# Performance work log

Measured on AMD Instinct MI355X. Metric: run time of the kernel, lower is better.

## Reference

```python
import jax, jax.numpy as jnp
import numpy as np

B, N, C_IN = 16, 1024, 768
H, KQ, VD = 8, 256, 512          # num_heads, kq_dim, v_dim per head
NH_V = H * VD                    # 4096
D_OUT = 512
SCALE = D_OUT ** -0.5            # module uses dim_out**-0.5
EPS = 1e-5


def _bn(x, gamma, beta, mean, var):
    # eval-mode BatchNorm1d over last dim
    return (x - mean) * (gamma * jax.lax.rsqrt(var + EPS)) + beta


def setup_inputs() -> dict:
    key = jax.random.key(0)
    ks = jax.random.split(key, 8)
    return {
        "x": jax.random.normal(ks[0], (B, N, C_IN), jnp.float32),
        "qkv_w": jax.random.normal(ks[1], (2 * H * KQ + NH_V, C_IN), jnp.float32) * 0.02,
        "qkv_gamma": jax.random.uniform(ks[2], (2 * H * KQ + NH_V,), jnp.float32),
        "qkv_beta": jax.random.normal(ks[3], (2 * H * KQ + NH_V,), jnp.float32) * 0.02,
        "qkv_mean": jax.random.normal(ks[4], (2 * H * KQ + NH_V,), jnp.float32) * 0.02,
        "qkv_var": jnp.ones((2 * H * KQ + NH_V,), jnp.float32),
        "pos_bias": jax.random.normal(ks[5], (H, N, N), jnp.float32),
        "proj_w": jax.random.normal(ks[6], (D_OUT, NH_V), jnp.float32) * 0.02,
        "proj_gamma": jax.random.uniform(ks[7], (D_OUT,), jnp.float32),
        "proj_beta": jnp.zeros((D_OUT,), jnp.float32),
        "proj_mean": jnp.zeros((D_OUT,), jnp.float32),
        "proj_var": jnp.ones((D_OUT,), jnp.float32),
    }


def reference(x, qkv_w, qkv_gamma, qkv_beta, qkv_mean, qkv_var,
              pos_bias, proj_w, proj_gamma, proj_beta, proj_mean, proj_var):
    b, n, _ = x.shape
    qkv = _bn(x @ qkv_w.T, qkv_gamma, qkv_beta, qkv_mean, qkv_var)  # [B,N,h]
    qkv = qkv.reshape(b, n, H, 2 * KQ + VD)
    q, k, v = jnp.split(qkv, [KQ, 2 * KQ], axis=3)                  # [B,N,H,*]
    attn = jnp.einsum('bnhd,bmhd->bhnm', q, k) * SCALE + pos_bias   # [B,H,N,N]
    attn = jax.nn.softmax(attn, axis=-1)
    out = jnp.einsum('bhnm,bmhd->bnhd', attn, v).reshape(b, n, NH_V)
    out = jnp.clip(out, -1.0, 1.0)                                  # Hardtanh
    return _bn(out @ proj_w.T, proj_gamma, proj_beta, proj_mean, proj_var)
```

## Files before the change

### kernel.cpp

```cpp
#include <hip/hip_runtime.h>

using v8bf  = __bf16 __attribute__((ext_vector_type(8)));
using v16f  = float  __attribute__((ext_vector_type(16)));

#define EPS_BN 1e-5f
#define ATT_SCALE 0.044194173824159216f
#define KSPLIT 2

__device__ __forceinline__ unsigned short f2bf(float f){
  union { float f; unsigned int u; } c; c.f = f;
  unsigned int u = c.u + 0x7fffu + ((c.u >> 16) & 1u);
  return (unsigned short)(u >> 16);
}

__device__ __forceinline__ v8bf ld8(const unsigned short* p){
  union { uint4 u; v8bf v; } c;
  c.u = *(const uint4*)p;
  return c.v;
}

__device__ __forceinline__ void glds16(const unsigned short* g, unsigned short* l){
  __builtin_amdgcn_global_load_lds(
      (const __attribute__((address_space(1))) void*)g,
      (__attribute__((address_space(3))) void*)l, 16, 0, 0);
}

__global__ void cast_bf16_kernel(const float* __restrict__ src,
                                 unsigned short* __restrict__ dst, int n8){
  int i = blockIdx.x * 256 + threadIdx.x;
  if (i >= n8) return;
  const float4* s4 = (const float4*)src;
  float4 a = s4[2*i], b = s4[2*i+1];
  union { unsigned short s[8]; uint4 u; } r;
  r.s[0]=f2bf(a.x); r.s[1]=f2bf(a.y); r.s[2]=f2bf(a.z); r.s[3]=f2bf(a.w);
  r.s[4]=f2bf(b.x); r.s[5]=f2bf(b.y); r.s[6]=f2bf(b.z); r.s[7]=f2bf(b.w);
  ((uint4*)dst)[i] = r.u;
}

__global__ void bn_precompute(const float* __restrict__ g, const float* __restrict__ be,
                              const float* __restrict__ mn, const float* __restrict__ vr,
                              float* __restrict__ scale, float* __restrict__ shift,
                              int n, int qfold){
  int i = blockIdx.x * 256 + threadIdx.x;
  if (i >= n) return;
  float s = g[i] * rsqrtf(vr[i] + EPS_BN);
  float t = be[i] - mn[i] * s;
  if (qfold && (i & 1023) < 256){ s *= ATT_SCALE; t *= ATT_SCALE; }
  scale[i] = s; shift[i] = t;
}

template<int MODE>
__launch_bounds__(256, 2)
__global__ void gemm_nt(const unsigned short* __restrict__ A,
                        const unsigned short* __restrict__ Bm,
                        int K, long sA, long sB, long mbase,
                        const float* __restrict__ scale, const float* __restrict__ shift,
                        const float* __restrict__ sums,
                        unsigned short* __restrict__ ob16,
                        float* __restrict__ outf,
                        unsigned short* __restrict__ vt)
{
  __shared__ __align__(16) unsigned short Sh[16384];
  unsigned short* As = Sh;
  unsigned short* Bs = Sh + 8192;
  const int tid = threadIdx.x;
  const int w = tid >> 6, lane = tid & 63, ln = lane & 31, lg = lane >> 5;
  const int wm = (w >> 1) * 64, wn = (w & 1) * 64;
  const long bm = (long)blockIdx.y * 128, bn = (long)blockIdx.x * 128;
  const int z = blockIdx.z;
  const unsigned short* Ab = A + (MODE == 3 ? 0L : (long)z * sA) + bm * K;
  const unsigned short* Bb = Bm + (MODE == 3 ? 0L : (long)z * sB) + bn * K;

  const int kbeg = (MODE == 3) ? z * (K >> 2) : 0;
  const int kend = (MODE == 3) ? kbeg + (K >> 2) : K;

  const int rsub = lane >> 3;
  const int gsl  = lane & 7;
  const unsigned short* gA[4]; const unsigned short* gB[4];
  unsigned short *lA[4], *lB[4];
  #pragma unroll
  for (int i = 0; i < 4; i++){
    int r = w*32 + i*8 + rsub;
    int go = (gsl ^ (r & 7)) * 8;
    gA[i] = Ab + (long)r * K + go;
    gB[i] = Bb + (long)r * K + go;
    lA[i] = As + (w*32 + i*8) * 64;
    lB[i] = Bs + (w*32 + i*8) * 64;
  }

  v16f acc[2][2];
  #pragma unroll
  for (int a = 0; a < 2; a++)
    #pragma unroll
    for (int b = 0; b < 2; b++)
      #pragma unroll
      for (int i = 0; i < 16; i++) acc[a][b][i] = 0.f;

  for (int k0 = kbeg; k0 < kend; k0 += 64){
    __syncthreads();
    #pragma unroll
    for (int i = 0; i < 4; i++){
      glds16(gA[i] + k0, lA[i]);
      glds16(gB[i] + k0, lB[i]);
    }
    __syncthreads();
    #pragma unroll
    for (int kk = 0; kk < 4; kk++){
      v8bf af[2], bfr[2];
      #pragma unroll
      for (int t = 0; t < 2; t++){
        int Ra = wm + t*32 + ln;
        af[t] = *(const v8bf*)&As[Ra*64 + ((kk*2 + lg) ^ (Ra & 7))*8];
        int Rb = wn + t*32 + ln;
        bfr[t] = *(const v8bf*)&Bs[Rb*64 + ((kk*2 + lg) ^ (Rb & 7))*8];
      }
      #pragma unroll
      for (int tm = 0; tm < 2; tm++)
        #pragma unroll
        for (int tn = 0; tn < 2; tn++)
          acc[tm][tn] = __builtin_amdgcn_mfma_f32_32x32x16_bf16(af[tm], bfr[tn], acc[tm][tn], 0, 0, 0);
    }
  }

  if (MODE == 0 && (blockIdx.x & 4)){
    __syncthreads();
    unsigned short* Ts = Sh;
    #pragma unroll
    for (int tm = 0; tm < 2; tm++){
      #pragma unroll
      for (int tn = 0; tn < 2; tn++){
        int c = wn + tn*32 + ln;
        long gn = bn + c;
        float sc = scale[gn], sh = shift[gn];
        int xk = (c & 15) << 3;
        #pragma unroll
        for (int q = 0; q < 4; q++){
          int mq = wm + tm*32 + 8*q + 4*lg;
          union { unsigned short s[4]; unsigned long long u; } pk;
          #pragma unroll
          for (int j = 0; j < 4; j++)
            pk.s[j] = f2bf(acc[tm][tn][q*4 + j] * sc + sh);
          *(unsigned long long*)&Ts[c*128 + (mq ^ xk)] = pk.u;
        }
      }
    }
    __syncthreads();
    const int h  = (int)(bn >> 10);
    const int j0 = (int)(bn & 1023) - 512;
    unsigned short* Vtb = vt + ((bm >> 10)*8 + h) * 524288L;
    const int nl0 = (int)(bm & 1023);
    #pragma unroll
    for (int i = 0; i < 8; i++){
      int idx = i*256 + tid;
      int c = idx >> 4, g = idx & 15;
      uint4 u = *(const uint4*)&Ts[c*128 + ((g ^ (c & 15)) << 3)];
      *(uint4*)(Vtb + (long)(j0 + c)*1024 + nl0 + g*8) = u;
    }
    return;
  }

  float invs[2][16];
  if (MODE == 1){
    #pragma unroll
    for (int tm = 0; tm < 2; tm++)
      #pragma unroll
      for (int i = 0; i < 16; i++){
        long gm = bm + wm + tm*32 + (i&3) + 8*(i>>2) + 4*lg;
        const float* sp = sums + (long)z * (KSPLIT*1024L) + gm;
        float s = 0.f;
        #pragma unroll
        for (int kp = 0; kp < KSPLIT; kp++) s += sp[kp*1024];
        invs[tm][i] = 1.0f / s;
      }
  }

  #pragma unroll
  for (int tm = 0; tm < 2; tm++){
    #pragma unroll
    for (int tn = 0; tn < 2; tn++){
      long gn = bn + wn + tn*32 + ln;
      float sc = 0.f, sh = 0.f;
      if (MODE == 0){ sc = scale[gn]; sh = shift[gn]; }
      #pragma unroll
      for (int i = 0; i < 16; i++){
        long gm = bm + wm + tm*32 + (i&3) + 8*(i>>2) + 4*lg;
        float v = acc[tm][tn][i];
        if (MODE == 0){
          ob16[gm*8192 + gn] = f2bf(v * sc + sh);
        } else if (MODE == 1){
          v = v * invs[tm][i];
          v = fminf(1.f, fmaxf(-1.f, v));
          int b2 = z >> 3, hh = z & 7;
          ob16[((long)b2*1024 + gm)*4096 + hh*512 + gn] = f2bf(v);
        } else {
          outf[((long)z * mbase + gm)*512 + gn] = v;
        }
      }
    }
  }
}

__global__ void reduce_bn(const float* __restrict__ part,
                          const float* __restrict__ sc, const float* __restrict__ sh,
                          float* __restrict__ out, long Mtot, long mbase){
  long idx = (long)blockIdx.x * 256 + threadIdx.x;
  if (idx >= Mtot * 128) return;
  long gm = idx >> 7;
  int gn4 = (int)(idx & 127) * 4;
  long PS = Mtot * 512;
  const float* p = part + gm*512 + gn4;
  float4 p0 = *(const float4*)(p);
  float4 p1 = *(const float4*)(p + PS);
  float4 p2 = *(const float4*)(p + 2*PS);
  float4 p3 = *(const float4*)(p + 3*PS);
  float4 s4 = *(const float4*)(sc + gn4);
  float4 h4 = *(const float4*)(sh + gn4);
  float4 r;
  r.x = (p0.x+p1.x+p2.x+p3.x)*s4.x + h4.x;
  r.y = (p0.y+p1.y+p2.y+p3.y)*s4.y + h4.y;
  r.z = (p0.z+p1.z+p2.z+p3.z)*s4.z + h4.z;
  r.w = (p0.w+p1.w+p2.w+p3.w)*s4.w + h4.w;
  *(float4*)(out + (mbase + gm)*512 + gn4) = r;
}

__launch_bounds__(256, 2)
__global__ void attn_scores(const unsigned short* __restrict__ qkv,
                            const float* __restrict__ bias,
                            unsigned short* __restrict__ E,
                            float* __restrict__ psums)
{
  __shared__ __align__(16) unsigned short Ks[2][64*256];
  const int lid  = blockIdx.x + (blockIdx.y << 4);
  const int xcd  = lid & 7;
  const int s_   = lid >> 3;
  const int mblk = s_ & 15;
  const int bh   = xcd + 8 * (s_ >> 4);
  const int b2 = bh >> 3, h = bh & 7;
  const int tid = threadIdx.x, w = tid >> 6, lane = tid & 63, ln = lane & 31, lg = lane >> 5;
  const int mh = w & 1, kh = w >> 1;
  const int m0 = mblk * 64 + mh * 32;
  const unsigned short* qbase = qkv + (long)b2*1024*8192 + h*1024;
  const unsigned short* kbase = qbase + 256;
  const float* biash = bias + (long)h * 1048576;
  unsigned short* Eb = E + (long)bh * 1048576;

  v8bf qf[16];
  {
    const unsigned short* qrow = qbase + (long)(m0 + ln)*8192 + lg*8;
    #pragma unroll
    for (int kf = 0; kf < 16; kf++) qf[kf] = ld8(qrow + kf*16);
  }

  const int rr = lane >> 5, slot = lane & 31;

  float sm[16];
  #pragma unroll
  for (int i = 0; i < 16; i++) sm[i] = 0.f;

  const int NT = 16;

  #pragma unroll
  for (int i = 0; i < 8; i++){
    int row = w*16 + i*2 + rr;
    glds16(kbase + (long)row*8192 + (slot ^ (row & 31))*8, &Ks[0][(w*16 + i*2)*256]);
  }

  for (int tt = 0; tt < NT; tt++){
    __syncthreads();
    const int cb = tt & 1;

    const int col = tt*64 + kh*32 + ln;
    float br[16];
    #pragma unroll
    for (int q = 0; q < 4; q++)
      #pragma unroll
      for (int j = 0; j < 4; j++)
        br[q*4 + j] = biash[(long)(m0 + 4*lg + 8*q + j)*1024 + col];

    if (tt < NT - 1){
      const int nb = cb ^ 1;
      #pragma unroll
      for (int i = 0; i < 8; i++){
        int row = w*16 + i*2 + rr;
        glds16(kbase + (long)((tt+1)*64 + row)*8192 + (slot ^ (row & 31))*8,
               &Ks[nb][(w*16 + i*2)*256]);
      }
    }

    v16f a[4];
    #pragma unroll
    for (int c = 0; c < 4; c++)
      #pragma unroll
      for (int i = 0; i < 16; i++) a[c][i] = 0.f;
    #pragma unroll
    for (int kb = 0; kb < 16; kb++){
      v8bf kf8 = *(const v8bf*)&Ks[cb][(kh*32 + ln)*256 + ((2*kb + lg) ^ ln)*8];
      a[kb & 3] = __builtin_amdgcn_mfma_f32_32x32x16_bf16(qf[kb], kf8, a[kb & 3], 0, 0, 0);
    }

    #pragma unroll
    for (int q = 0; q < 4; q++){
      #pragma unroll
      for (int j = 0; j < 4; j++){
        int i = q*4 + j;
        int r = 4*lg + 8*q + j;
        float e = __expf((a[0][i] + a[1][i]) + (a[2][i] + a[3][i]) + br[i]);
        sm[i] += e;
        Eb[(long)(m0 + r)*1024 + col] = f2bf(e);
      }
    }
  }

  #pragma unroll
  for (int i = 0; i < 16; i++){
    #pragma unroll
    for (int d = 1; d < 32; d <<= 1) sm[i] += __shfl_xor(sm[i], d, 64);
  }
  if (ln == 0){
    float* sp = psums + ((long)bh * KSPLIT + kh)*1024 + m0 + 4*lg;
    #pragma unroll
    for (int q = 0; q < 4; q++)
      #pragma unroll
      for (int j = 0; j < 4; j++)
        sp[8*q + j] = sm[q*4 + j];
  }
}

extern "C" void kernel_launch(void* const* d_in, const int* in_sizes, int n_in,
                              void* d_out, int out_size, void* d_ws, size_t ws_size,
                              hipStream_t stream)
{
  const float* x        = (const float*)d_in[0];
  const float* qkv_w    = (const float*)d_in[1];
  const float* qg       = (const float*)d_in[2];
  const float* qb       = (const float*)d_in[3];
  const float* qm       = (const float*)d_in[4];
  const float* qv       = (const float*)d_in[5];
  const float* pos_bias = (const float*)d_in[6];
  const float* pw       = (const float*)d_in[7];
  const float* pg       = (const float*)d_in[8];
  const float* pbt      = (const float*)d_in[9];
  const float* pmn      = (const float*)d_in[10];
  const float* pvr      = (const float*)d_in[11];
  float* out = (float*)d_out;

  const unsigned long FIXED = 16846848UL;
  const unsigned long PERG  = 43548672UL;
  long G = 1;
  if      (ws_size >= FIXED + PERG*16) G = 16;
  else if (ws_size >= FIXED + PERG*8)  G = 8;
  else if (ws_size >= FIXED + PERG*4)  G = 4;
  else if (ws_size >= FIXED + PERG*2)  G = 2;
  else if (ws_size >= FIXED + PERG)    G = 1;
  else return;

  char* ws = (char*)d_ws;
  unsigned short* wqb = (unsigned short*)(ws + 0L);
  unsigned short* wpb = (unsigned short*)(ws + 12582912L);
  float* sc_qkv       = (float*)(ws + 16777216L);
  float* sh_qkv       = (float*)(ws + 16809984L);
  float* sc_p         = (float*)(ws + 16842752L);
  float* sh_p         = (float*)(ws + 16844800L);
  const long gb = 16846848L;
  unsigned short* xbg   = (unsigned short*)(ws + gb);
  unsigned short* qkvg  = (unsigned short*)(ws + gb + G*1572864L);
  unsigned short* Vtg   = (unsigned short*)(ws + gb + G*18350080L);
  unsigned short* Eg    = (unsigned short*)(ws + gb + G*26738688L);
  float* sumsg          = (float*)(ws + gb + G*43515904L);
  unsigned short* outcg = qkvg;
  float* partials       = (float*)Eg;
  float* psums          = (float*)xbg;
  (void)sumsg;

  cast_bf16_kernel<<<dim3(3072), 256, 0, stream>>>(qkv_w, wqb, 786432);
  cast_bf16_kernel<<<dim3(1024), 256, 0, stream>>>(pw,    wpb, 262144);
  bn_precompute<<<dim3(32), 256, 0, stream>>>(qg, qb, qm, qv, sc_qkv, sh_qkv, 8192, 1);
  bn_precompute<<<dim3(2),  256, 0, stream>>>(pg, pbt, pmn, pvr, sc_p, sh_p, 512, 0);

  const int nG = (int)(16 / G);
  for (int g = 0; g < nG; g++){
    const float* xg = x + (long)g * G * 786432L;
    long mbase = (long)g * G * 1024L;

    cast_bf16_kernel<<<dim3((unsigned)(G*384)), 256, 0, stream>>>(xg, xbg, (int)(G*98304));

    gemm_nt<0><<<dim3(64, (unsigned)(8*G), 1), 256, 0, stream>>>(
        xbg, wqb, 768, 0L, 0L, 0L, sc_qkv, sh_qkv, nullptr, qkvg, nullptr, Vtg);

    attn_scores<<<dim3(16, (unsigned)(8*G)), 256, 0, stream>>>(
        qkvg, pos_bias, Eg, psums);

    gemm_nt<1><<<dim3(4, 8, (unsigned)(8*G)), 256, 0, stream>>>(
        Eg, Vtg, 1024, 1048576L, 524288L, 0L, nullptr, nullptr, psums, outcg, nullptr, nullptr);

    gemm_nt<3><<<dim3(4, (unsigned)(8*G), 4), 256, 0, stream>>>(
        outcg, wpb, 4096, 0L, 0L, (long)(G*1024), nullptr, nullptr, nullptr,
        nullptr, partials, nullptr);

    reduce_bn<<<dim3((unsigned)(G*512)), 256, 0, stream>>>(
        partials, sc_p, sh_p, out, (long)(G*1024), mbase);
  }
}
```

Baseline: 979.5 us.

## Double-buffer LDS tiles in gemm_nt to overlap global loads with MFMA

```diff
diff --git a/kernel.cpp b/kernel.cpp
--- a/kernel.cpp
+++ b/kernel.cpp
@@ -60,9 +60,7 @@
                         float* __restrict__ outf,
                         unsigned short* __restrict__ vt)
 {
-  __shared__ __align__(16) unsigned short Sh[16384];
-  unsigned short* As = Sh;
-  unsigned short* Bs = Sh + 8192;
+  __shared__ __align__(16) unsigned short Sh[32768];
   const int tid = threadIdx.x;
   const int w = tid >> 6, lane = tid & 63, ln = lane & 31, lg = lane >> 5;
   const int wm = (w >> 1) * 64, wn = (w & 1) * 64;
@@ -77,15 +75,14 @@
   const int rsub = lane >> 3;
   const int gsl  = lane & 7;
   const unsigned short* gA[4]; const unsigned short* gB[4];
-  unsigned short *lA[4], *lB[4];
+  int lofs[4];
   #pragma unroll
   for (int i = 0; i < 4; i++){
     int r = w*32 + i*8 + rsub;
     int go = (gsl ^ (r & 7)) * 8;
     gA[i] = Ab + (long)r * K + go;
     gB[i] = Bb + (long)r * K + go;
-    lA[i] = As + (w*32 + i*8) * 64;
-    lB[i] = Bs + (w*32 + i*8) * 64;
+    lofs[i] = (w*32 + i*8) * 64;
   }
 
   v16f acc[2][2];
@@ -96,23 +93,35 @@
       #pragma unroll
       for (int i = 0; i < 16; i++) acc[a][b][i] = 0.f;
 
+  #pragma unroll
+  for (int i = 0; i < 4; i++){
+    glds16(gA[i] + kbeg, Sh + lofs[i]);
+    glds16(gB[i] + kbeg, Sh + 16384 + lofs[i]);
+  }
+  asm volatile("s_waitcnt vmcnt(0) lgkmcnt(0)" ::: "memory");
+  __builtin_amdgcn_s_barrier();
+
+  int cur = 0;
   for (int k0 = kbeg; k0 < kend; k0 += 64){
-    __syncthreads();
-    #pragma unroll
-    for (int i = 0; i < 4; i++){
-      glds16(gA[i] + k0, lA[i]);
-      glds16(gB[i] + k0, lB[i]);
-    }
-    __syncthreads();
+    if (k0 + 64 < kend){
+      const int nb = cur ^ 1;
+      #pragma unroll
+      for (int i = 0; i < 4; i++){
+        glds16(gA[i] + k0 + 64, Sh + nb*8192 + lofs[i]);
+        glds16(gB[i] + k0 + 64, Sh + 16384 + nb*8192 + lofs[i]);
+      }
+    }
+    const unsigned short* Ac = Sh + cur*8192;
+    const unsigned short* Bc = Sh + 16384 + cur*8192;
     #pragma unroll
     for (int kk = 0; kk < 4; kk++){
       v8bf af[2], bfr[2];
       #pragma unroll
       for (int t = 0; t < 2; t++){
         int Ra = wm + t*32 + ln;
-        af[t] = *(const v8bf*)&As[Ra*64 + ((kk*2 + lg) ^ (Ra & 7))*8];
+        af[t] = *(const v8bf*)&Ac[Ra*64 + ((kk*2 + lg) ^ (Ra & 7))*8];
         int Rb = wn + t*32 + ln;
-        bfr[t] = *(const v8bf*)&Bs[Rb*64 + ((kk*2 + lg) ^ (Rb & 7))*8];
+        bfr[t] = *(const v8bf*)&Bc[Rb*64 + ((kk*2 + lg) ^ (Rb & 7))*8];
       }
       #pragma unroll
       for (int tm = 0; tm < 2; tm++)
@@ -120,10 +129,12 @@
         for (int tn = 0; tn < 2; tn++)
           acc[tm][tn] = __builtin_amdgcn_mfma_f32_32x32x16_bf16(af[tm], bfr[tn], acc[tm][tn], 0, 0, 0);
     }
+    asm volatile("s_waitcnt vmcnt(0) lgkmcnt(0)" ::: "memory");
+    __builtin_amdgcn_s_barrier();
+    cur ^= 1;
   }
 
   if (MODE == 0 && (blockIdx.x & 4)){
-    __syncthreads();
     unsigned short* Ts = Sh;
     #pragma unroll
     for (int tm = 0; tm < 2; tm++){
```

Measured after the change: 1.003 ms. 1.02x slower.

## Halve K-tile LDS staging in attn_scores to raise occupancy to four blocks

Applied to the files above, without the earlier changes.

```diff
diff --git a/kernel.cpp b/kernel.cpp
--- a/kernel.cpp
+++ b/kernel.cpp
@@ -223,13 +223,13 @@
   *(float4*)(out + (mbase + gm)*512 + gn4) = r;
 }
 
-__launch_bounds__(256, 2)
+__launch_bounds__(256, 4)
 __global__ void attn_scores(const unsigned short* __restrict__ qkv,
                             const float* __restrict__ bias,
                             unsigned short* __restrict__ E,
                             float* __restrict__ psums)
 {
-  __shared__ __align__(16) unsigned short Ks[2][64*256];
+  __shared__ __align__(16) unsigned short Ks[2][64*128];
   const int lid  = blockIdx.x + (blockIdx.y << 4);
   const int xcd  = lid & 7;
   const int s_   = lid >> 3;
@@ -251,62 +251,60 @@
     for (int kf = 0; kf < 16; kf++) qf[kf] = ld8(qrow + kf*16);
   }
 
-  const int rr = lane >> 5, slot = lane & 31;
+  const int r4  = lane >> 4;
+  const int s16 = lane & 15;
 
   float sm[16];
   #pragma unroll
   for (int i = 0; i < 16; i++) sm[i] = 0.f;
 
-  const int NT = 16;
-
-  #pragma unroll
-  for (int i = 0; i < 8; i++){
-    int row = w*16 + i*2 + rr;
-    glds16(kbase + (long)row*8192 + (slot ^ (row & 31))*8, &Ks[0][(w*16 + i*2)*256]);
-  }
-
-  for (int tt = 0; tt < NT; tt++){
+  auto stage = [&](int s, int buf){
+    int t = s >> 1, hf = s & 1;
+    const unsigned short* src0 = kbase + (long)(t*64)*8192 + hf*128;
+    #pragma unroll
+    for (int i = 0; i < 4; i++){
+      int row = w*16 + i*4 + r4;
+      glds16(src0 + (long)row*8192 + (s16 ^ (row & 15))*8,
+             &Ks[buf][(w*16 + i*4)*128]);
+    }
+  };
+
+  stage(0, 0);
+
+  v16f a[2];
+
+  for (int s = 0; s < 32; s++){
     __syncthreads();
-    const int cb = tt & 1;
-
-    const int col = tt*64 + kh*32 + ln;
-    float br[16];
-    #pragma unroll
-    for (int q = 0; q < 4; q++)
-      #pragma unroll
-      for (int j = 0; j < 4; j++)
-        br[q*4 + j] = biash[(long)(m0 + 4*lg + 8*q + j)*1024 + col];
-
-    if (tt < NT - 1){
-      const int nb = cb ^ 1;
-      #pragma unroll
-      for (int i = 0; i < 8; i++){
-        int row = w*16 + i*2 + rr;
-        glds16(kbase + (long)((tt+1)*64 + row)*8192 + (slot ^ (row & 31))*8,
-               &Ks[nb][(w*16 + i*2)*256]);
-      }
-    }
-
-    v16f a[4];
-    #pragma unroll
-    for (int c = 0; c < 4; c++)
-      #pragma unroll
-      for (int i = 0; i < 16; i++) a[c][i] = 0.f;
-    #pragma unroll
-    for (int kb = 0; kb < 16; kb++){
-      v8bf kf8 = *(const v8bf*)&Ks[cb][(kh*32 + ln)*256 + ((2*kb + lg) ^ ln)*8];
-      a[kb & 3] = __builtin_amdgcn_mfma_f32_32x32x16_bf16(qf[kb], kf8, a[kb & 3], 0, 0, 0);
-    }
-
-    #pragma unroll
-    for (int q = 0; q < 4; q++){
-      #pragma unroll
-      for (int j = 0; j < 4; j++){
-        int i = q*4 + j;
-        int r = 4*lg + 8*q + j;
-        float e = __expf((a[0][i] + a[1][i]) + (a[2][i] + a[3][i]) + br[i]);
-        sm[i] += e;
-        Eb[(long)(m0 + r)*1024 + col] = f2bf(e);
+    const int cb = s & 1;
+    const int t = s >> 1, hf = s & 1;
+
+    if (hf == 0){
+      #pragma unroll
+      for (int c = 0; c < 2; c++)
+        #pragma unroll
+        for (int i = 0; i < 16; i++) a[c][i] = 0.f;
+    }
+
+    if (s < 31) stage(s + 1, cb ^ 1);
+
+    #pragma unroll
+    for (int kb = 0; kb < 8; kb++){
+      v8bf kf8 = *(const v8bf*)&Ks[cb][(kh*32 + ln)*128 + ((2*kb + lg) ^ (ln & 15))*8];
+      a[kb & 1] = __builtin_amdgcn_mfma_f32_32x32x16_bf16(qf[hf*8 + kb], kf8, a[kb & 1], 0, 0, 0);
+    }
+
+    if (hf == 1){
+      const int col = t*64 + kh*32 + ln;
+      #pragma unroll
+      for (int q = 0; q < 4; q++){
+        #pragma unroll
+        for (int j = 0; j < 4; j++){
+          int i = q*4 + j;
+          int r = 4*lg + 8*q + j;
+          float e = __expf(a[0][i] + a[1][i] + biash[(long)(m0 + r)*1024 + col]);
+          sm[i] += e;
+          Eb[(long)(m0 + r)*1024 + col] = f2bf(e);
+        }
       }
     }
   }
```

Result: slower. 1.620 ms (+65.4%).

## Fuse attention scores, softmax normalization and PV matmul into one kernel

Applied to the files above, without the earlier changes.

```diff
diff --git a/kernel.cpp b/kernel.cpp
--- a/kernel.cpp
+++ b/kernel.cpp
@@ -5,7 +5,6 @@
 
 #define EPS_BN 1e-5f
 #define ATT_SCALE 0.044194173824159216f
-#define KSPLIT 2
 
 __device__ __forceinline__ unsigned short f2bf(float f){
   union { float f; unsigned int u; } c; c.f = f;
@@ -55,7 +54,6 @@
                         const unsigned short* __restrict__ Bm,
                         int K, long sA, long sB, long mbase,
                         const float* __restrict__ scale, const float* __restrict__ shift,
-                        const float* __restrict__ sums,
                         unsigned short* __restrict__ ob16,
                         float* __restrict__ outf,
                         unsigned short* __restrict__ vt)
@@ -159,21 +157,6 @@
     return;
   }
 
-  float invs[2][16];
-  if (MODE == 1){
-    #pragma unroll
-    for (int tm = 0; tm < 2; tm++)
-      #pragma unroll
-      for (int i = 0; i < 16; i++){
-        long gm = bm + wm + tm*32 + (i&3) + 8*(i>>2) + 4*lg;
-        const float* sp = sums + (long)z * (KSPLIT*1024L) + gm;
-        float s = 0.f;
-        #pragma unroll
-        for (int kp = 0; kp < KSPLIT; kp++) s += sp[kp*1024];
-        invs[tm][i] = 1.0f / s;
-      }
-  }
-
   #pragma unroll
   for (int tm = 0; tm < 2; tm++){
     #pragma unroll
@@ -187,11 +170,6 @@
         float v = acc[tm][tn][i];
         if (MODE == 0){
           ob16[gm*8192 + gn] = f2bf(v * sc + sh);
-        } else if (MODE == 1){
-          v = v * invs[tm][i];
-          v = fminf(1.f, fmaxf(-1.f, v));
-          int b2 = z >> 3, hh = z & 7;
-          ob16[((long)b2*1024 + gm)*4096 + hh*512 + gn] = f2bf(v);
         } else {
           outf[((long)z * mbase + gm)*512 + gn] = v;
         }
@@ -224,40 +202,46 @@
 }
 
 __launch_bounds__(256, 2)
-__global__ void attn_scores(const unsigned short* __restrict__ qkv,
-                            const float* __restrict__ bias,
-                            unsigned short* __restrict__ E,
-                            float* __restrict__ psums)
+__global__ void attn_fused(const unsigned short* __restrict__ qkv,
+                           const float* __restrict__ bias,
+                           const unsigned short* __restrict__ Vt,
+                           unsigned short* __restrict__ outc)
 {
   __shared__ __align__(16) unsigned short Ks[2][64*256];
-  const int lid  = blockIdx.x + (blockIdx.y << 4);
+  __shared__ __align__(16) unsigned short Ps[32*72];
+  __shared__ float sums_lds[2][32];
+
+  const int lid  = blockIdx.x + (blockIdx.y << 5);
   const int xcd  = lid & 7;
   const int s_   = lid >> 3;
-  const int mblk = s_ & 15;
-  const int bh   = xcd + 8 * (s_ >> 4);
+  const int mblk = s_ & 31;
+  const int bh   = xcd + 8 * (s_ >> 5);
   const int b2 = bh >> 3, h = bh & 7;
   const int tid = threadIdx.x, w = tid >> 6, lane = tid & 63, ln = lane & 31, lg = lane >> 5;
-  const int mh = w & 1, kh = w >> 1;
-  const int m0 = mblk * 64 + mh * 32;
+  const int m0 = mblk * 32;
   const unsigned short* qbase = qkv + (long)b2*1024*8192 + h*1024;
   const unsigned short* kbase = qbase + 256;
   const float* biash = bias + (long)h * 1048576;
-  unsigned short* Eb = E + (long)bh * 1048576;
+  const unsigned short* Vb = Vt + (long)bh * 524288;
+
+  const int rr = lane >> 5, slot = lane & 31;
 
   v8bf qf[16];
-  {
+  if (w < 2){
     const unsigned short* qrow = qbase + (long)(m0 + ln)*8192 + lg*8;
     #pragma unroll
     for (int kf = 0; kf < 16; kf++) qf[kf] = ld8(qrow + kf*16);
   }
 
-  const int rr = lane >> 5, slot = lane & 31;
-
   float sm[16];
   #pragma unroll
   for (int i = 0; i < 16; i++) sm[i] = 0.f;
 
-  const int NT = 16;
+  v16f acc[4];
+  #pragma unroll
+  for (int nb = 0; nb < 4; nb++)
+    #pragma unroll
+    for (int i = 0; i < 16; i++) acc[nb][i] = 0.f;
 
   #pragma unroll
   for (int i = 0; i < 8; i++){
@@ -265,48 +249,64 @@
     glds16(kbase + (long)row*8192 + (slot ^ (row & 31))*8, &Ks[0][(w*16 + i*2)*256]);
   }
 
-  for (int tt = 0; tt < NT; tt++){
-    __syncthreads();
+  for (int tt = 0; tt < 16; tt++){
     const int cb = tt & 1;
-
-    const int col = tt*64 + kh*32 + ln;
-    float br[16];
-    #pragma unroll
-    for (int q = 0; q < 4; q++)
-      #pragma unroll
-      for (int j = 0; j < 4; j++)
-        br[q*4 + j] = biash[(long)(m0 + 4*lg + 8*q + j)*1024 + col];
-
-    if (tt < NT - 1){
-      const int nb = cb ^ 1;
+    __syncthreads();
+
+    if (w < 2){
+      const int kh = w;
+      const int col = tt*64 + kh*32 + ln;
+      float br[16];
+      #pragma unroll
+      for (int q = 0; q < 4; q++)
+        #pragma unroll
+        for (int j = 0; j < 4; j++)
+          br[q*4 + j] = biash[(long)(m0 + 4*lg + 8*q + j)*1024 + col];
+
+      v16f a0, a1;
+      #pragma unroll
+      for (int i = 0; i < 16; i++){ a0[i] = 0.f; a1[i] = 0.f; }
+      #pragma unroll
+      for (int kb = 0; kb < 16; kb += 2){
+        v8bf k0 = *(const v8bf*)&Ks[cb][(kh*32 + ln)*256 + ((2*kb     + lg) ^ ln)*8];
+        v8bf k1 = *(const v8bf*)&Ks[cb][(kh*32 + ln)*256 + ((2*kb + 2 + lg) ^ ln)*8];
+        a0 = __builtin_amdgcn_mfma_f32_32x32x16_bf16(qf[kb],   k0, a0, 0, 0, 0);
+        a1 = __builtin_amdgcn_mfma_f32_32x32x16_bf16(qf[kb+1], k1, a1, 0, 0, 0);
+      }
+      #pragma unroll
+      for (int q = 0; q < 4; q++){
+        #pragma unroll
+        for (int j = 0; j < 4; j++){
+          int i = q*4 + j;
+          int r = 4*lg + 8*q + j;
+          float e = __expf(a0[i] + a1[i] + br[i]);
+          sm[i] += e;
+          Ps[r*72 + kh*32 + ln] = f2bf(e);
+        }
+      }
+    }
+    __syncthreads();
+
+    if (tt < 15){
       #pragma unroll
       for (int i = 0; i < 8; i++){
         int row = w*16 + i*2 + rr;
         glds16(kbase + (long)((tt+1)*64 + row)*8192 + (slot ^ (row & 31))*8,
-               &Ks[nb][(w*16 + i*2)*256]);
-      }
-    }
-
-    v16f a[4];
-    #pragma unroll
-    for (int c = 0; c < 4; c++)
-      #pragma unroll
-      for (int i = 0; i < 16; i++) a[c][i] = 0.f;
-    #pragma unroll
-    for (int kb = 0; kb < 16; kb++){
-      v8bf kf8 = *(const v8bf*)&Ks[cb][(kh*32 + ln)*256 + ((2*kb + lg) ^ ln)*8];
-      a[kb & 3] = __builtin_amdgcn_mfma_f32_32x32x16_bf16(qf[kb], kf8, a[kb & 3], 0, 0, 0);
-    }
-
-    #pragma unroll
-    for (int q = 0; q < 4; q++){
-      #pragma unroll
-      for (int j = 0; j < 4; j++){
-        int i = q*4 + j;
-        int r = 4*lg + 8*q + j;
-        float e = __expf((a[0][i] + a[1][i]) + (a[2][i] + a[3][i]) + br[i]);
-        sm[i] += e;
-        Eb[(long)(m0 + r)*1024 + col] = f2bf(e);
+               &Ks[cb ^ 1][(w*16 + i*2)*256]);
+      }
+    }
+
+    v8bf pf[4];
+    #pragma unroll
+    for (int ks = 0; ks < 4; ks++)
+      pf[ks] = *(const v8bf*)&Ps[ln*72 + ks*16 + lg*8];
+    #pragma unroll
+    for (int nb = 0; nb < 4; nb++){
+      const unsigned short* vrow = Vb + (long)(w*128 + nb*32 + ln)*1024 + tt*64 + lg*8;
+      #pragma unroll
+      for (int ks = 0; ks < 4; ks++){
+        v8bf vf = ld8(vrow + ks*16);
+        acc[nb] = __builtin_amdgcn_mfma_f32_32x32x16_bf16(pf[ks], vf, acc[nb], 0, 0, 0);
       }
     }
   }
@@ -316,13 +316,32 @@
     #pragma unroll
     for (int d = 1; d < 32; d <<= 1) sm[i] += __shfl_xor(sm[i], d, 64);
   }
-  if (ln == 0){
-    float* sp = psums + ((long)bh * KSPLIT + kh)*1024 + m0 + 4*lg;
+  if (w < 2 && ln == 0){
     #pragma unroll
     for (int q = 0; q < 4; q++)
       #pragma unroll
       for (int j = 0; j < 4; j++)
-        sp[8*q + j] = sm[q*4 + j];
+        sums_lds[w][4*lg + 8*q + j] = sm[q*4 + j];
+  }
+  __syncthreads();
+
+  float invs[16];
+  #pragma unroll
+  for (int i = 0; i < 16; i++){
+    int r = 4*lg + 8*(i>>2) + (i&3);
+    invs[i] = 1.0f / (sums_lds[0][r] + sums_lds[1][r]);
+  }
+
+  unsigned short* ob = outc + ((long)b2*1024 + m0)*4096 + h*512 + w*128;
+  #pragma unroll
+  for (int nb = 0; nb < 4; nb++){
+    #pragma unroll
+    for (int i = 0; i < 16; i++){
+      int r = 4*lg + 8*(i>>2) + (i&3);
+      float v = acc[nb][i] * invs[i];
+      v = fminf(1.f, fmaxf(-1.f, v));
+      ob[(long)r*4096 + nb*32 + ln] = f2bf(v);
+    }
   }
 }
 
@@ -365,12 +384,8 @@
   unsigned short* xbg   = (unsigned short*)(ws + gb);
   unsigned short* qkvg  = (unsigned short*)(ws + gb + G*1572864L);
   unsigned short* Vtg   = (unsigned short*)(ws + gb + G*18350080L);
-  unsigned short* Eg    = (unsigned short*)(ws + gb + G*26738688L);
-  float* sumsg          = (float*)(ws + gb + G*43515904L);
-  unsigned short* outcg = qkvg;
-  float* partials       = (float*)Eg;
-  float* psums          = (float*)xbg;
-  (void)sumsg;
+  unsigned short* outcg = (unsigned short*)(ws + gb + G*26738688L);
+  float* partials       = (float*)(ws + gb + G*26738688L + G*8388608L);
 
   cast_bf16_kernel<<<dim3(3072), 256, 0, stream>>>(qkv_w, wqb, 786432);
   cast_bf16_kernel<<<dim3(1024), 256, 0, stream>>>(pw,    wpb, 262144);
@@ -385,16 +400,13 @@
     cast_bf16_kernel<<<dim3((unsigned)(G*384)), 256, 0, stream>>>(xg, xbg, (int)(G*98304));
 
     gemm_nt<0><<<dim3(64, (unsigned)(8*G), 1), 256, 0, stream>>>(
-        xbg, wqb, 768, 0L, 0L, 0L, sc_qkv, sh_qkv, nullptr, qkvg, nullptr, Vtg);
-
-    attn_scores<<<dim3(16, (unsigned)(8*G)), 256, 0, stream>>>(
-        qkvg, pos_bias, Eg, psums);
-
-    gemm_nt<1><<<dim3(4, 8, (unsigned)(8*G)), 256, 0, stream>>>(
-        Eg, Vtg, 1024, 1048576L, 524288L, 0L, nullptr, nullptr, psums, outcg, nullptr, nullptr);
+        xbg, wqb, 768, 0L, 0L, 0L, sc_qkv, sh_qkv, qkvg, nullptr, Vtg);
+
+    attn_fused<<<dim3(32, (unsigned)(8*G)), 256, 0, stream>>>(
+        qkvg, pos_bias, Vtg, outcg);
 
     gemm_nt<3><<<dim3(4, (unsigned)(8*G), 4), 256, 0, stream>>>(
-        outcg, wpb, 4096, 0L, 0L, (long)(G*1024), nullptr, nullptr, nullptr,
+        outcg, wpb, 4096, 0L, 0L, (long)(G*1024), nullptr, nullptr,
         nullptr, partials, nullptr);
 
     reduce_bn<<<dim3((unsigned)(G*512)), 256, 0, stream>>>(
```

New measurement: 1.491 ms. +52.2%, slower.
